# Kernel tuning notes

Measured on AMD Instinct MI355X. Metric: run time of the kernel, lower is better.

Reference implementation:

```python
import jax, jax.numpy as jnp
import numpy as np
from jax import lax

CHUNK = 256  # query chunk size (manual tiling block)

def setup_inputs() -> dict:
    key = jax.random.key(0)
    kq, kk, kv = jax.random.split(key, 3)
    shape = (2, 16, 2048, 128)  # [B, H, S, D]
    q = jax.random.normal(kq, shape, dtype=jnp.float32)
    k = jax.random.normal(kk, shape, dtype=jnp.float32)
    v = jax.random.normal(kv, shape, dtype=jnp.float32)
    return {"q": q, "k": k, "v": v}

def reference(q, k, v):
    # Chunked (memory-efficient) exact attention: softmax(QK^T/sqrt(D)) V,
    # computed one query block at a time so the full [S,S] score matrix
    # is never materialized.
    B, H, S, D = q.shape
    scale = jnp.asarray(1.0 / np.sqrt(D), dtype=q.dtype)
    n_chunks = S // CHUNK
    # [n_chunks, B, H, CHUNK, D]
    q_blocks = q.reshape(B, H, n_chunks, CHUNK, D).transpose(2, 0, 1, 3, 4)

    def step(carry, q_blk):
        # scores for this query block vs all keys: [B, H, CHUNK, S]
        s = jnp.einsum('bhqd,bhkd->bhqk', q_blk, k) * scale
        p = jax.nn.softmax(s, axis=-1)
        o = jnp.einsum('bhqk,bhkd->bhqd', p, v)
        return carry, o

    _, out_blocks = lax.scan(step, None, q_blocks)
    # [n_chunks, B, H, CHUNK, D] -> [B, H, S, D]
    out = out_blocks.transpose(1, 2, 0, 3, 4).reshape(B, H, S, D)
    return out
```

## Files before the change

### kernel.cpp

```cpp
#include <hip/hip_runtime.h>
#include <hip/hip_bf16.h>


typedef short short8 __attribute__((ext_vector_type(8)));
typedef float f32x16 __attribute__((ext_vector_type(16)));

#define MFMA32(a, b, c) __builtin_amdgcn_mfma_f32_32x32x16_bf16((a), (b), (c), 0, 0, 0)

#if __has_builtin(__builtin_amdgcn_exp2f)
#define EXP2(x) __builtin_amdgcn_exp2f(x)
#else
#define EXP2(x) exp2f(x)
#endif

constexpr int Dh  = 128;
constexpr int S_  = 2048;
constexpr int KVB = 64;
constexpr int NT  = S_ / KVB;
constexpr int WAVES = 8;
constexpr int QBLK  = 256;

__device__ __forceinline__ short f2bf(float f) {
    union { float f; unsigned u; } x; x.f = f;
    unsigned r = x.u + 0x7fffu + ((x.u >> 16) & 1u);
    return (short)(r >> 16);
}

__device__ __forceinline__ unsigned pkbf(float lo, float hi) {
    unsigned r;
    asm("v_cvt_pk_bf16_f32 %0, %1, %2" : "=v"(r) : "v"(lo), "v"(hi));
    return r;
}

__device__ __forceinline__ void gload16(const void* g, void* l) {
    __builtin_amdgcn_global_load_lds(
        (const __attribute__((address_space(1))) unsigned int*)g,
        (__attribute__((address_space(3))) unsigned int*)l, 16, 0, 0);
}

__global__ __launch_bounds__(256) void prep_k(const float* __restrict__ K,
                                              short* __restrict__ Kz) {
    int idx = blockIdx.x * 256 + threadIdx.x;
    int b   = idx & 15;
    int s   = (idx >> 4) & (S_ - 1);
    int sb  = b ^ (s & 15);
    const float* src = K + (size_t)(idx >> 4) * Dh + sb * 8;
    float4 f0 = ((const float4*)src)[0];
    float4 f1 = ((const float4*)src)[1];
    short8 o;
    o[0] = f2bf(f0.x); o[1] = f2bf(f0.y); o[2] = f2bf(f0.z); o[3] = f2bf(f0.w);
    o[4] = f2bf(f1.x); o[5] = f2bf(f1.y); o[6] = f2bf(f1.z); o[7] = f2bf(f1.w);
    *(short8*)(Kz + (size_t)idx * 8) = o;
}

__global__ __launch_bounds__(256) void prep_v(const float* __restrict__ V,
                                              short* __restrict__ Vt) {
    __shared__ short tr[64][72];
    int bid = blockIdx.x;
    int dg = bid & 1, seg = (bid >> 1) & 31, bh = bid >> 6;
    int t = threadIdx.x;
    int s = t >> 2, d0 = (t & 3) * 16;
    const float* src = V + (size_t)(bh * S_ + seg * 64 + s) * Dh + dg * 64 + d0;
    #pragma unroll
    for (int i = 0; i < 16; i += 4) {
        float4 f = *(const float4*)(src + i);
        tr[d0 + i + 0][s] = f2bf(f.x); tr[d0 + i + 1][s] = f2bf(f.y);
        tr[d0 + i + 2][s] = f2bf(f.z); tr[d0 + i + 3][s] = f2bf(f.w);
    }
    __syncthreads();
    int d = t >> 2, j0 = (t & 3) * 2;
    size_t ob = ((size_t)(bh * 32 + seg) * 128 + dg * 64 + d) * 64;
    #pragma unroll
    for (int jj = 0; jj < 2; ++jj) {
        int j = j0 + jj;
        int sj = (j ^ (d & 7)) * 8;
        short8 val = *(const short8*)&tr[d][sj];
        *(short8*)(Vt + ob + j * 8) = val;
    }
}

__global__ __launch_bounds__(512, 2)
void mea_fwd4(const float* __restrict__ Qg, const short* __restrict__ Kz,
              const short* __restrict__ Vt, float* __restrict__ Og, int nqt) {
    __shared__ __align__(16) short k0[KVB * Dh], k1[KVB * Dh];
    __shared__ __align__(16) short v0[Dh * KVB], v1[Dh * KVB];
    __shared__ float bc_lds[WAVES][32];

    const int bid = blockIdx.x;
    const int cpx = (int)gridDim.x >> 3;
    const int swz = (bid & 7) * cpx + (bid >> 3);
    const int qt  = swz % nqt;
    const int bh  = swz / nqt;

    const int tid  = threadIdx.x;
    const int w    = tid >> 6;
    const int lane = tid & 63;
    const int l31  = lane & 31;
    const int hi   = lane >> 5;

    const size_t base = (size_t)bh * S_ * Dh;
    const int    qrow = qt * QBLK + w * 32 + l31;
    const float  QSC  = 0.08838834764831845f * 1.4426950408889634f;

    short8 qf[8];
    {
        const float* qp = Qg + base + (size_t)qrow * Dh;
        #pragma unroll
        for (int kc = 0; kc < 8; ++kc) {
            const float4 f0 = *(const float4*)(qp + kc * 16 + hi * 8);
            const float4 f1 = *(const float4*)(qp + kc * 16 + hi * 8 + 4);
            short8 a;
            a[0] = f2bf(f0.x * QSC); a[1] = f2bf(f0.y * QSC);
            a[2] = f2bf(f0.z * QSC); a[3] = f2bf(f0.w * QSC);
            a[4] = f2bf(f1.x * QSC); a[5] = f2bf(f1.y * QSC);
            a[6] = f2bf(f1.z * QSC); a[7] = f2bf(f1.w * QSC);
            qf[kc] = a;
        }
    }

    f32x16 oacc[4];
    #pragma unroll
    for (int dt = 0; dt < 4; ++dt)
        #pragma unroll
        for (int r = 0; r < 16; ++r) oacc[dt][r] = 0.f;
    float mrun = -1e30f, lpart = 0.f;

    const short* kt0 = Kz + base;
    const short* vt0 = Vt + base;

    auto STAGE = [&](short* kl, short* vl, int t) {
        const short* ks = kt0 + (size_t)t * (KVB * Dh);
        const short* vs = vt0 + (size_t)t * (Dh * KVB);
        #pragma unroll
        for (int i = 0; i < 2; ++i) {
            const int ou = (i * 8 + w) * 512;
            gload16(ks + ou + lane * 8, kl + ou);
            gload16(vs + ou + lane * 8, vl + ou);
        }
    };

    auto COMPUTE = [&](const short* kl, const short* vl) {
        f32x16 sa, sb;
        #pragma unroll
        for (int r = 0; r < 16; ++r) { sa[r] = 0.f; sb[r] = 0.f; }
        __builtin_amdgcn_s_setprio(1);
        #pragma unroll
        for (int kc = 0; kc < 8; ++kc) {
            const int go = (((kc * 2 + hi) ^ (l31 & 15)) * 8);
            const short8 a0 = *(const short8*)&kl[l31 * Dh + go];
            const short8 a1 = *(const short8*)&kl[(32 + l31) * Dh + go];
            sa = MFMA32(a0, qf[kc], sa);
            sb = MFMA32(a1, qf[kc], sb);
        }
        __builtin_amdgcn_s_setprio(0);

        float mxl = sa[0];
        #pragma unroll
        for (int r = 1; r < 16; ++r) mxl = fmaxf(mxl, sa[r]);
        #pragma unroll
        for (int r = 0; r < 16; ++r) mxl = fmaxf(mxl, sb[r]);
        if (__any(mxl > mrun + 8.0f)) {
            float mo   = fmaxf(mxl, __shfl_xor(mxl, 32));
            float mnew = fmaxf(mrun, mo);
            float rc   = EXP2(mrun - mnew);
            mrun = mnew;
            lpart *= rc;
            if (!hi) bc_lds[w][l31] = rc;
            #pragma unroll
            for (int m = 0; m < 4; ++m) {
                const float4 rcv = *(const float4*)&bc_lds[w][m * 8 + 4 * hi];
                #pragma unroll
                for (int t2 = 0; t2 < 4; ++t2) {
                    const float f = (&rcv.x)[t2];
                    #pragma unroll
                    for (int dt = 0; dt < 4; ++dt) oacc[dt][m * 4 + t2] *= f;
                }
            }
        }

        f32x16 pa, pb;
        float s0 = 0.f, s1 = 0.f;
        #pragma unroll
        for (int r = 0; r < 16; ++r) { pa[r] = EXP2(sa[r] - mrun); s0 += pa[r]; }
        #pragma unroll
        for (int r = 0; r < 16; ++r) { pb[r] = EXP2(sb[r] - mrun); s1 += pb[r]; }
        lpart += s0 + s1;

        short8 pf[4];
        #pragma unroll
        for (int ks = 0; ks < 4; ++ks) {
            const int qA = (ks & 1) * 2, qB = qA + 1;
            float eA0, eA1, eA2, eA3, eB0, eB1, eB2, eB3;
            if (ks < 2) {
                eA0 = pa[qA*4+0]; eA1 = pa[qA*4+1]; eA2 = pa[qA*4+2]; eA3 = pa[qA*4+3];
                eB0 = pa[qB*4+0]; eB1 = pa[qB*4+1]; eB2 = pa[qB*4+2]; eB3 = pa[qB*4+3];
            } else {
                eA0 = pb[qA*4+0]; eA1 = pb[qA*4+1]; eA2 = pb[qA*4+2]; eA3 = pb[qA*4+3];
                eB0 = pb[qB*4+0]; eB1 = pb[qB*4+1]; eB2 = pb[qB*4+2]; eB3 = pb[qB*4+3];
            }
            const unsigned uA0 = pkbf(eA0, eA1), uA1 = pkbf(eA2, eA3);
            const unsigned uB0 = pkbf(eB0, eB1), uB1 = pkbf(eB2, eB3);
            const unsigned y0 = hi ? uA0 : uB0;
            const unsigned y1 = hi ? uA1 : uB1;
            const unsigned r0 = (unsigned)__shfl_xor((int)y0, 32);
            const unsigned r1 = (unsigned)__shfl_xor((int)y1, 32);
            unsigned wd[4];
            wd[0] = hi ? r0 : uA0;  wd[1] = hi ? r1 : uA1;
            wd[2] = hi ? uB0 : r0;  wd[3] = hi ? uB1 : r1;
            pf[ks] = *(const short8*)wd;
        }

        __builtin_amdgcn_s_setprio(1);
        #pragma unroll
        for (int dt = 0; dt < 4; ++dt) {
            #pragma unroll
            for (int ks = 0; ks < 4; ++ks) {
                const short8 bv = *(const short8*)
                    &vl[(dt * 32 + l31) * KVB + (((ks * 2 + hi) ^ (l31 & 7)) * 8)];
                oacc[dt] = MFMA32(pf[ks], bv, oacc[dt]);
            }
        }
        __builtin_amdgcn_s_setprio(0);
    };

    STAGE(k0, v0, 0);
    __syncthreads();
    #pragma unroll 1
    for (int t = 0; t < NT; t += 2) {
        STAGE(k1, v1, t + 1);
        COMPUTE(k0, v0);
        __syncthreads();
        if (t + 2 < NT) STAGE(k0, v0, t + 2);
        COMPUTE(k1, v1);
        __syncthreads();
    }

    {
        const float tot = lpart + __shfl_xor(lpart, 32);
        if (!hi) bc_lds[w][l31] = 1.0f / tot;
    }
    float* op = Og + base;
    #pragma unroll
    for (int m = 0; m < 4; ++m) {
        const float4 li = *(const float4*)&bc_lds[w][m * 8 + 4 * hi];
        #pragma unroll
        for (int t2 = 0; t2 < 4; ++t2) {
            const int row  = m * 8 + 4 * hi + t2;
            const float lf = (&li.x)[t2];
            #pragma unroll
            for (int dt = 0; dt < 4; ++dt)
                op[(size_t)(qt * QBLK + w * 32 + row) * Dh + dt * 32 + l31]
                    = oacc[dt][m * 4 + t2] * lf;
        }
    }
}

typedef float f32x4 __attribute__((ext_vector_type(4)));
#define MFMA16(a, b, c) __builtin_amdgcn_mfma_f32_16x16x32_bf16((a), (b), (c), 0, 0, 0)
constexpr int FKVB = 32;
constexpr int FKP  = 136;
constexpr int FVP  = 40;
constexpr int FPP  = 40;

__global__ __launch_bounds__(256, 2)
void mea_fwd_fb(const float* __restrict__ Qg, const float* __restrict__ Kg,
                const float* __restrict__ Vg, float* __restrict__ Og,
                int S, int nqt) {
    __shared__ __align__(16) short k_lds[FKVB][FKP];
    __shared__ __align__(16) short vT_lds[Dh][FVP];
    __shared__ __align__(16) short p_lds[4][16][FPP];

    const int qt = blockIdx.x % nqt;
    const int bh = blockIdx.x / nqt;
    const int tid = threadIdx.x;
    const int w = tid >> 6, lane = tid & 63;
    const int lr = lane & 15, lg = lane >> 4;
    const size_t base = (size_t)bh * S * Dh;
    const int qrow0 = qt * 64 + w * 16;
    const float scale = 0.08838834764831845f;

    short8 qf[4];
    {
        const float* qp = Qg + base + (size_t)(qrow0 + lr) * Dh;
        #pragma unroll
        for (int kc = 0; kc < 4; ++kc) {
            const float4 f0 = *(const float4*)(qp + kc * 32 + lg * 8);
            const float4 f1 = *(const float4*)(qp + kc * 32 + lg * 8 + 4);
            short8 a;
            a[0] = f2bf(f0.x); a[1] = f2bf(f0.y); a[2] = f2bf(f0.z); a[3] = f2bf(f0.w);
            a[4] = f2bf(f1.x); a[5] = f2bf(f1.y); a[6] = f2bf(f1.z); a[7] = f2bf(f1.w);
            qf[kc] = a;
        }
    }
    f32x4 oacc[8];
    #pragma unroll
    for (int dt = 0; dt < 8; ++dt) oacc[dt] = (f32x4){0.f, 0.f, 0.f, 0.f};
    float mrun[4] = {-1e30f, -1e30f, -1e30f, -1e30f};
    float lrun[4] = {0.f, 0.f, 0.f, 0.f};
    const int sr = tid >> 3, sc = (tid & 7) * 16;

    for (int kv0 = 0; kv0 < S; kv0 += FKVB) {
        {
            const float* kp = Kg + base + (size_t)(kv0 + sr) * Dh + sc;
            const float* vp = Vg + base + (size_t)(kv0 + sr) * Dh + sc;
            short8 pk0, pk1;
            float4 f0 = ((const float4*)kp)[0], f1 = ((const float4*)kp)[1];
            float4 f2 = ((const float4*)kp)[2], f3 = ((const float4*)kp)[3];
            pk0[0] = f2bf(f0.x); pk0[1] = f2bf(f0.y); pk0[2] = f2bf(f0.z); pk0[3] = f2bf(f0.w);
            pk0[4] = f2bf(f1.x); pk0[5] = f2bf(f1.y); pk0[6] = f2bf(f1.z); pk0[7] = f2bf(f1.w);
            pk1[0] = f2bf(f2.x); pk1[1] = f2bf(f2.y); pk1[2] = f2bf(f2.z); pk1[3] = f2bf(f2.w);
            pk1[4] = f2bf(f3.x); pk1[5] = f2bf(f3.y); pk1[6] = f2bf(f3.z); pk1[7] = f2bf(f3.w);
            *(short8*)&k_lds[sr][sc] = pk0;
            *(short8*)&k_lds[sr][sc + 8] = pk1;
            #pragma unroll
            for (int i = 0; i < 4; ++i) {
                float4 f = ((const float4*)vp)[i];
                vT_lds[sc + 4 * i + 0][sr] = f2bf(f.x);
                vT_lds[sc + 4 * i + 1][sr] = f2bf(f.y);
                vT_lds[sc + 4 * i + 2][sr] = f2bf(f.z);
                vT_lds[sc + 4 * i + 3][sr] = f2bf(f.w);
            }
        }
        __syncthreads();
        f32x4 s0 = (f32x4){0.f,0.f,0.f,0.f}, s1 = (f32x4){0.f,0.f,0.f,0.f};
        #pragma unroll
        for (int kc = 0; kc < 4; ++kc) {
            short8 b0 = *(const short8*)&k_lds[lr][kc * 32 + lg * 8];
            short8 b1 = *(const short8*)&k_lds[16 + lr][kc * 32 + lg * 8];
            s0 = MFMA16(qf[kc], b0, s0);
            s1 = MFMA16(qf[kc], b1, s1);
        }
        float resc[4];
        #pragma unroll
        for (int r = 0; r < 4; ++r) {
            float mxv = fmaxf(s0[r], s1[r]);
            #pragma unroll
            for (int m = 1; m < 16; m <<= 1) mxv = fmaxf(mxv, __shfl_xor(mxv, m));
            float mnew = fmaxf(mrun[r], mxv * scale);
            float rc = __expf(mrun[r] - mnew);
            mrun[r] = mnew;
            float p0 = __expf(s0[r] * scale - mnew);
            float p1 = __expf(s1[r] * scale - mnew);
            float rs = p0 + p1;
            #pragma unroll
            for (int m = 1; m < 16; m <<= 1) rs += __shfl_xor(rs, m);
            lrun[r] = lrun[r] * rc + rs;
            resc[r] = rc;
            p_lds[w][lg * 4 + r][lr] = f2bf(p0);
            p_lds[w][lg * 4 + r][16 + lr] = f2bf(p1);
        }
        #pragma unroll
        for (int dt = 0; dt < 8; ++dt) {
            f32x4 o = oacc[dt];
            o[0] *= resc[0]; o[1] *= resc[1]; o[2] *= resc[2]; o[3] *= resc[3];
            oacc[dt] = o;
        }
        short8 ap = *(const short8*)&p_lds[w][lr][lg * 8];
        #pragma unroll
        for (int dt = 0; dt < 8; ++dt) {
            short8 bv = *(const short8*)&vT_lds[dt * 16 + lr][lg * 8];
            oacc[dt] = MFMA16(ap, bv, oacc[dt]);
        }
        __syncthreads();
    }
    float inv[4];
    #pragma unroll
    for (int r = 0; r < 4; ++r) inv[r] = 1.0f / lrun[r];
    float* op = Og + base;
    #pragma unroll
    for (int dt = 0; dt < 8; ++dt)
        #pragma unroll
        for (int r = 0; r < 4; ++r)
            op[(size_t)(qrow0 + lg * 4 + r) * Dh + dt * 16 + lr] = oacc[dt][r] * inv[r];
}

extern "C" void kernel_launch(void* const* d_in, const int* in_sizes, int n_in,
                              void* d_out, int out_size, void* d_ws, size_t ws_size,
                              hipStream_t stream) {
    const float* q = (const float*)d_in[0];
    const float* k = (const float*)d_in[1];
    const float* v = (const float*)d_in[2];
    float* o = (float*)d_out;

    const int BH  = in_sizes[0] / (S_ * Dh);
    const int nqt = S_ / QBLK;

    const size_t kz_bytes = (size_t)BH * S_ * Dh * sizeof(short);
    const size_t need = 2 * kz_bytes;

    if (ws_size >= need) {
        short* Kz = (short*)d_ws;
        short* Vt = (short*)((char*)d_ws + kz_bytes);
        hipLaunchKernelGGL(prep_k, dim3(BH * S_ * 16 / 256), dim3(256), 0, stream, k, Kz);
        hipLaunchKernelGGL(prep_v, dim3(BH * (S_ / 64) * 2), dim3(256), 0, stream, v, Vt);
        hipLaunchKernelGGL(mea_fwd4, dim3(BH * nqt), dim3(512), 0, stream, q, Kz, Vt, o, nqt);
    } else {
        hipLaunchKernelGGL(mea_fwd_fb, dim3(BH * (S_ / 64)), dim3(256), 0, stream,
                           q, k, v, o, S_, S_ / 64);
    }
}
```

Before: 96.71 us.

## Halve query block to 4 waves and use permlane32 swap for P packing

Shrinks the attention kernel's work-group from 8 to 4 waves and the query block from 256 to 128 rows. This doubles the grid and the number of K/V tile loads per query, with each wave now staging four 16-byte chunks per tile. It also replaces the shfl_xor-plus-select exchange used to build the bf16 P operand with v_permlane32_swap on packed pairs, which cuts cross-lane shuffle and select work. The trade-off is less K/V reuse per block and more total global traffic, in exchange for more blocks to fill the CUs and cheaper softmax-to-MFMA repacking.

```diff
diff --git a/kernel.cpp b/kernel.cpp
--- a/kernel.cpp
+++ b/kernel.cpp
@@ -17,8 +17,8 @@
 constexpr int S_  = 2048;
 constexpr int KVB = 64;
 constexpr int NT  = S_ / KVB;
-constexpr int WAVES = 8;
-constexpr int QBLK  = 256;
+constexpr int WAVES = 4;
+constexpr int QBLK  = 128;
 
 __device__ __forceinline__ short f2bf(float f) {
     union { float f; unsigned u; } x; x.f = f;
@@ -30,6 +30,10 @@
     unsigned r;
     asm("v_cvt_pk_bf16_f32 %0, %1, %2" : "=v"(r) : "v"(lo), "v"(hi));
     return r;
+}
+
+__device__ __forceinline__ void pswap(unsigned &a, unsigned &b) {
+    asm("v_permlane32_swap_b32 %0, %1" : "+v"(a), "+v"(b));
 }
 
 __device__ __forceinline__ void gload16(const void* g, void* l) {
@@ -79,8 +83,8 @@
     }
 }
 
-__global__ __launch_bounds__(512, 2)
-void mea_fwd4(const float* __restrict__ Qg, const short* __restrict__ Kz,
+__global__ __launch_bounds__(256, 2)
+void mea_fwd5(const float* __restrict__ Qg, const short* __restrict__ Kz,
               const short* __restrict__ Vt, float* __restrict__ Og, int nqt) {
     __shared__ __align__(16) short k0[KVB * Dh], k1[KVB * Dh];
     __shared__ __align__(16) short v0[Dh * KVB], v1[Dh * KVB];
@@ -132,8 +136,8 @@
         const short* ks = kt0 + (size_t)t * (KVB * Dh);
         const short* vs = vt0 + (size_t)t * (Dh * KVB);
         #pragma unroll
-        for (int i = 0; i < 2; ++i) {
-            const int ou = (i * 8 + w) * 512;
+        for (int i = 0; i < 4; ++i) {
+            const int ou = (i * 4 + w) * 512;
             gload16(ks + ou + lane * 8, kl + ou);
             gload16(vs + ou + lane * 8, vl + ou);
         }
@@ -187,27 +191,27 @@
         lpart += s0 + s1;
 
         short8 pf[4];
-        #pragma unroll
-        for (int ks = 0; ks < 4; ++ks) {
-            const int qA = (ks & 1) * 2, qB = qA + 1;
-            float eA0, eA1, eA2, eA3, eB0, eB1, eB2, eB3;
-            if (ks < 2) {
-                eA0 = pa[qA*4+0]; eA1 = pa[qA*4+1]; eA2 = pa[qA*4+2]; eA3 = pa[qA*4+3];
-                eB0 = pa[qB*4+0]; eB1 = pa[qB*4+1]; eB2 = pa[qB*4+2]; eB3 = pa[qB*4+3];
-            } else {
-                eA0 = pb[qA*4+0]; eA1 = pb[qA*4+1]; eA2 = pb[qA*4+2]; eA3 = pb[qA*4+3];
-                eB0 = pb[qB*4+0]; eB1 = pb[qB*4+1]; eB2 = pb[qB*4+2]; eB3 = pb[qB*4+3];
+        {
+            #pragma unroll
+            for (int kk = 0; kk < 2; ++kk) {
+                unsigned a0 = pkbf(pa[kk * 8 + 0], pa[kk * 8 + 1]);
+                unsigned a1 = pkbf(pa[kk * 8 + 2], pa[kk * 8 + 3]);
+                unsigned b0 = pkbf(pa[kk * 8 + 4], pa[kk * 8 + 5]);
+                unsigned b1 = pkbf(pa[kk * 8 + 6], pa[kk * 8 + 7]);
+                pswap(a0, b0); pswap(a1, b1);
+                unsigned wd[4] = {a0, a1, b0, b1};
+                pf[kk] = *(const short8*)wd;
             }
-            const unsigned uA0 = pkbf(eA0, eA1), uA1 = pkbf(eA2, eA3);
-            const unsigned uB0 = pkbf(eB0, eB1), uB1 = pkbf(eB2, eB3);
-            const unsigned y0 = hi ? uA0 : uB0;
-            const unsigned y1 = hi ? uA1 : uB1;
-            const unsigned r0 = (unsigned)__shfl_xor((int)y0, 32);
-            const unsigned r1 = (unsigned)__shfl_xor((int)y1, 32);
-            unsigned wd[4];
-            wd[0] = hi ? r0 : uA0;  wd[1] = hi ? r1 : uA1;
-            wd[2] = hi ? uB0 : r0;  wd[3] = hi ? uB1 : r1;
-            pf[ks] = *(const short8*)wd;
+            #pragma unroll
+            for (int kk = 0; kk < 2; ++kk) {
+                unsigned a0 = pkbf(pb[kk * 8 + 0], pb[kk * 8 + 1]);
+                unsigned a1 = pkbf(pb[kk * 8 + 2], pb[kk * 8 + 3]);
+                unsigned b0 = pkbf(pb[kk * 8 + 4], pb[kk * 8 + 5]);
+                unsigned b1 = pkbf(pb[kk * 8 + 6], pb[kk * 8 + 7]);
+                pswap(a0, b0); pswap(a1, b1);
+                unsigned wd[4] = {a0, a1, b0, b1};
+                pf[2 + kk] = *(const short8*)wd;
+            }
         }
 
         __builtin_amdgcn_s_setprio(1);
@@ -393,7 +397,7 @@
         short* Vt = (short*)((char*)d_ws + kz_bytes);
         hipLaunchKernelGGL(prep_k, dim3(BH * S_ * 16 / 256), dim3(256), 0, stream, k, Kz);
         hipLaunchKernelGGL(prep_v, dim3(BH * (S_ / 64) * 2), dim3(256), 0, stream, v, Vt);
-        hipLaunchKernelGGL(mea_fwd4, dim3(BH * nqt), dim3(512), 0, stream, q, Kz, Vt, o, nqt);
+        hipLaunchKernelGGL(mea_fwd5, dim3(BH * nqt), dim3(256), 0, stream, q, Kz, Vt, o, nqt);
     } else {
         hipLaunchKernelGGL(mea_fwd_fb, dim3(BH * (S_ / 64)), dim3(256), 0, stream,
                            q, k, v, o, S_, S_ / 64);
```

After: 97.32 us. About the same (+0.6%).
